# Kernel tuning notes

Hardware: AMD Instinct MI355X
Metric: run time of the kernel (lower is better)

## Reference

```python
import jax, jax.numpy as jnp
import numpy as np
import math

B, S, D, H = 2, 2048, 1024, 16
DK = D // H


def setup_inputs() -> dict:
    key = jax.random.key(0)
    ks = jax.random.split(key, 8)
    scale = 0.02
    f = lambda k, shape: jax.random.normal(k, shape, dtype=jnp.float32)
    causal = jnp.tril(jnp.ones((S, S), dtype=jnp.int32))  # [S,S]
    mask = jnp.broadcast_to(causal[None, None], (B, 1, S, S))
    return {
        "query": f(ks[0], (B, S, D)),
        "key_in": f(ks[1], (B, S, D)),
        "value": f(ks[2], (B, S, D)),
        "Wq": f(ks[3], (D, D)) * scale, "bq": jnp.zeros((D,), jnp.float32),
        "Wk": f(ks[4], (D, D)) * scale, "bk": jnp.zeros((D,), jnp.float32),
        "Wv": f(ks[5], (D, D)) * scale, "bv": jnp.zeros((D,), jnp.float32),
        "Wo": f(ks[6], (D, D)) * scale, "bo": jnp.zeros((D,), jnp.float32),
        "mask": mask,
    }


def reference(query, key_in, value, Wq, bq, Wk, bk, Wv, bv, Wo, bo, mask):
    # linear projections (torch Linear: x @ W.T + b), split into heads -> [B,H,S,DK]
    def proj(x, W, b):
        return (x @ W.T + b).reshape(B, -1, H, DK).transpose(0, 2, 1, 3)

    q = proj(query, Wq, bq)
    k = proj(key_in, Wk, bk)
    v = proj(value, Wv, bv)

    scores = jnp.einsum("bhqd,bhkd->bhqk", q, k) / math.sqrt(DK)  # [B,H,S,S]
    scores = jnp.where(mask.astype(bool), scores, -jnp.inf)
    attn = jax.nn.softmax(scores, axis=-1)
    x = jnp.einsum("bhqk,bhkd->bhqd", attn, v)  # [B,H,S,DK]
    x = x.transpose(0, 2, 1, 3).reshape(B, S, D)
    return x @ Wo.T + bo
```

## Files before the change

### kernel.cpp

```cpp
#include <hip/hip_runtime.h>
#include <hip/hip_bf16.h>

constexpr int Bc = 2, Sc = 2048, Dc = 1024, Hc = 16, DKc = 64;
constexpr int Nrows = Bc * Sc;

typedef short bf16x8 __attribute__((ext_vector_type(8)));
typedef float floatx4 __attribute__((ext_vector_type(4)));
typedef unsigned short u16x8 __attribute__((ext_vector_type(8)));

__device__ __forceinline__ short f2bf(float f) {
    union { float f; unsigned u; } v; v.f = f;
    unsigned r = v.u + 0x7FFFu + ((v.u >> 16) & 1u);
    return (short)(r >> 16);
}

__device__ __forceinline__ void gld16(const void* g, void* l) {
    __builtin_amdgcn_global_load_lds((const __attribute__((address_space(1))) unsigned int*)g,
                                     (__attribute__((address_space(3))) unsigned int*)l,
                                     16, 0, 0);
}

__global__ __launch_bounds__(256) void cvt_bf16(
        const float* __restrict__ s0, const float* __restrict__ s1, const float* __restrict__ s2,
        const float* __restrict__ s3, const float* __restrict__ s4, const float* __restrict__ s5,
        const float* __restrict__ s6,
        short* __restrict__ d0, short* __restrict__ d1, short* __restrict__ d2,
        short* __restrict__ d3, short* __restrict__ d4, short* __restrict__ d5,
        short* __restrict__ d6) {
    const float* src; short* dst; int n;
    switch (blockIdx.y) {
        case 0: src = s0; dst = d0; n = Nrows * Dc; break;
        case 1: src = s1; dst = d1; n = Nrows * Dc; break;
        case 2: src = s2; dst = d2; n = Nrows * Dc; break;
        case 3: src = s3; dst = d3; n = Dc * Dc; break;
        case 4: src = s4; dst = d4; n = Dc * Dc; break;
        case 5: src = s5; dst = d5; n = Dc * Dc; break;
        default: src = s6; dst = d6; n = Dc * Dc; break;
    }
    const int stride = gridDim.x * 256 * 8;
    for (int i = (blockIdx.x * 256 + threadIdx.x) * 8; i < n; i += stride) {
        const float4 a = *(const float4*)(src + i);
        const float4 b = *(const float4*)(src + i + 4);
        u16x8 o;
        o[0] = (unsigned short)f2bf(a.x); o[1] = (unsigned short)f2bf(a.y);
        o[2] = (unsigned short)f2bf(a.z); o[3] = (unsigned short)f2bf(a.w);
        o[4] = (unsigned short)f2bf(b.x); o[5] = (unsigned short)f2bf(b.y);
        o[6] = (unsigned short)f2bf(b.z); o[7] = (unsigned short)f2bf(b.w);
        *(u16x8*)(dst + i) = o;
    }
}

template <int BM>
__device__ __forceinline__ void gemm_body(const short* __restrict__ A,
                                          const short* __restrict__ W,
                                          const float* __restrict__ bias,
                                          void* __restrict__ Cout,
                                          int mode, short* As, short* Ws) {
    constexpr int K = Dc, BK = 64;
    constexpr int MB = BM / 16;
    constexpr int A_BLKS = MB * 2;
    constexpr int TOT = A_BLKS + 16;
    constexpr int PER_W = TOT / 4;
    constexpr int WMB = MB / 2;

    const int tid  = threadIdx.x;
    const int w    = tid >> 6;
    const int lane = tid & 63;
    const int quad = lane >> 4;
    const int l15  = lane & 15;
    const int rowBase = blockIdx.y * BM;
    const int colBase = blockIdx.x * 128;
    const int wm = w >> 1, wn = w & 1;

    floatx4 acc[WMB][4];
#pragma unroll
    for (int j = 0; j < WMB; ++j)
#pragma unroll
        for (int t = 0; t < 4; ++t) acc[j][t] = (floatx4){0.f, 0.f, 0.f, 0.f};

    for (int k0 = 0; k0 < K; k0 += BK) {
        __syncthreads();
#pragma unroll
        for (int i = 0; i < PER_W; ++i) {
            const int blk = w * PER_W + i;
            if (blk < A_BLKS) {
                const int mb = blk >> 1, kh = blk & 1;
                const short* g = A + (size_t)(rowBase + mb * 16 + l15) * K + k0 + kh * 32 + quad * 8;
                gld16(g, As + blk * 512);
            } else {
                const int b2 = blk - A_BLKS;
                const int nb = b2 >> 1, kh = b2 & 1;
                const short* g = W + (size_t)(colBase + nb * 16 + l15) * K + k0 + kh * 32 + quad * 8;
                gld16(g, Ws + b2 * 512);
            }
        }
        __syncthreads();

        bf16x8 af[WMB][2], wf[4][2];
#pragma unroll
        for (int j = 0; j < WMB; ++j)
#pragma unroll
            for (int kh = 0; kh < 2; ++kh)
                af[j][kh] = *(const bf16x8*)(As + ((wm * WMB + j) * 2 + kh) * 512 + lane * 8);
#pragma unroll
        for (int t = 0; t < 4; ++t)
#pragma unroll
            for (int kh = 0; kh < 2; ++kh)
                wf[t][kh] = *(const bf16x8*)(Ws + ((wn * 4 + t) * 2 + kh) * 512 + lane * 8);

#pragma unroll
        for (int kh = 0; kh < 2; ++kh)
#pragma unroll
            for (int j = 0; j < WMB; ++j)
#pragma unroll
                for (int t = 0; t < 4; ++t)
                    acc[j][t] = __builtin_amdgcn_mfma_f32_16x16x32_bf16(af[j][kh], wf[t][kh], acc[j][t], 0, 0, 0);
    }

#pragma unroll
    for (int j = 0; j < WMB; ++j) {
#pragma unroll
        for (int t = 0; t < 4; ++t) {
            const int col = colBase + wn * 64 + t * 16 + l15;
            const float bv = bias[col];
            const int row0 = rowBase + (wm * WMB + j) * 16 + quad * 4;
            if (mode == 0) {
                float* Co = (float*)Cout;
#pragma unroll
                for (int r = 0; r < 4; ++r)
                    Co[(size_t)(row0 + r) * Dc + col] = acc[j][t][r] + bv;
            } else {
                short* Co = (short*)Cout;
                const int b = row0 >> 11;
                const int ss0 = row0 & (Sc - 1);
                const int h = col >> 6, dk = col & 63;
                if (mode == 1) {
#pragma unroll
                    for (int r = 0; r < 4; ++r)
                        Co[(((size_t)(b * Hc + h)) * Sc + ss0 + r) * DKc + dk] = f2bf(acc[j][t][r] + bv);
                } else {
                    short4 pk;
                    pk.x = f2bf(acc[j][t][0] + bv); pk.y = f2bf(acc[j][t][1] + bv);
                    pk.z = f2bf(acc[j][t][2] + bv); pk.w = f2bf(acc[j][t][3] + bv);
                    *(short4*)(Co + (((size_t)(b * Hc + h)) * DKc + dk) * Sc + ss0) = pk;
                }
            }
        }
    }
}

__global__ __launch_bounds__(256) void gemm_qkv(
        const short* __restrict__ Aq, const short* __restrict__ Ak, const short* __restrict__ Av,
        const short* __restrict__ Wq, const short* __restrict__ Wk, const short* __restrict__ Wv,
        const float* __restrict__ bq, const float* __restrict__ bk, const float* __restrict__ bv,
        short* __restrict__ Oq, short* __restrict__ Ok, short* __restrict__ Ov) {
    __shared__ short As[128 * 64];
    __shared__ short Ws[128 * 64];
    const int z = blockIdx.z;
    const short* A = (z == 0) ? Aq : (z == 1) ? Ak : Av;
    const short* W = (z == 0) ? Wq : (z == 1) ? Wk : Wv;
    const float* bs = (z == 0) ? bq : (z == 1) ? bk : bv;
    short* O = (z == 0) ? Oq : (z == 1) ? Ok : Ov;
    gemm_body<128>(A, W, bs, O, (z == 2) ? 2 : 1, As, Ws);
}

__global__ __launch_bounds__(256) void gemm_out(const short* __restrict__ A,
                                                const short* __restrict__ W,
                                                const float* __restrict__ bias,
                                                float* __restrict__ C) {
    __shared__ short As[64 * 64];
    __shared__ short Ws[128 * 64];
    gemm_body<64>(A, W, bias, C, 0, As, Ws);
}

__global__ __launch_bounds__(256) void flash_attn_mfma(const short* __restrict__ Qg,
                                                       const short* __restrict__ Kg,
                                                       const short* __restrict__ Vtg,
                                                       short* __restrict__ X) {
    constexpr int LD = 88;
    __shared__ short Kt[64 * LD];
    __shared__ short Vl[64 * LD];
    __shared__ short Pl[4 * 16 * LD];

    const int bh = blockIdx.x;
    const int qt = blockIdx.y;
    const int tid  = threadIdx.x;
    const int w    = tid >> 6;
    const int lane = tid & 63;
    const int quad = lane >> 4;
    const int l15  = lane & 15;

    const short* Qb = Qg  + (size_t)bh * Sc * DKc;
    const short* Kb = Kg  + (size_t)bh * Sc * DKc;
    const short* Vb = Vtg + (size_t)bh * DKc * Sc;

    bf16x8 qf[2];
    {
        const short* qp = Qb + (size_t)(qt * 64 + w * 16 + l15) * DKc + quad * 8;
        qf[0] = *(const bf16x8*)(qp);
        qf[1] = *(const bf16x8*)(qp + 32);
    }

    floatx4 oacc[4];
#pragma unroll
    for (int t = 0; t < 4; ++t) oacc[t] = (floatx4){0.f, 0.f, 0.f, 0.f};
    float m_run[4], l_run[4];
#pragma unroll
    for (int r = 0; r < 4; ++r) { m_run[r] = -1e30f; l_run[r] = 0.f; }

    short* Pw = Pl + w * 16 * LD;

    for (int kt = 0; kt <= qt; ++kt) {
        __syncthreads();
#pragma unroll
        for (int i = 0; i < 2; ++i) {
            const int c = tid + 256 * i;
            const int ky = c >> 3, d8 = (c & 7) * 8;
            *(uint4*)&Kt[ky * LD + d8] = *(const uint4*)(Kb + (size_t)(kt * 64 + ky) * DKc + d8);
        }
#pragma unroll
        for (int i = 0; i < 2; ++i) {
            const int c = tid + 256 * i;
            const int dk = c >> 3, k8 = (c & 7) * 8;
            *(uint4*)&Vl[dk * LD + k8] = *(const uint4*)(Vb + (size_t)dk * Sc + kt * 64 + k8);
        }
        __syncthreads();

        floatx4 sacc[4];
#pragma unroll
        for (int t = 0; t < 4; ++t) sacc[t] = (floatx4){0.f, 0.f, 0.f, 0.f};
#pragma unroll
        for (int t = 0; t < 4; ++t)
#pragma unroll
            for (int kh = 0; kh < 2; ++kh) {
                const bf16x8 kf = *(const bf16x8*)&Kt[(t * 16 + l15) * LD + kh * 32 + quad * 8];
                sacc[t] = __builtin_amdgcn_mfma_f32_16x16x32_bf16(qf[kh], kf, sacc[t], 0, 0, 0);
            }

        const bool diag = (kt == qt);
#pragma unroll
        for (int t = 0; t < 4; ++t)
#pragma unroll
            for (int r = 0; r < 4; ++r) {
                float s = sacc[t][r] * 0.125f;
                if (diag && (t * 16 + l15) > (w * 16 + quad * 4 + r)) s = -1e30f;
                sacc[t][r] = s;
            }

        float mt[4];
#pragma unroll
        for (int r = 0; r < 4; ++r)
            mt[r] = fmaxf(fmaxf(sacc[0][r], sacc[1][r]), fmaxf(sacc[2][r], sacc[3][r]));
#pragma unroll
        for (int off = 1; off < 16; off <<= 1)
#pragma unroll
            for (int r = 0; r < 4; ++r) mt[r] = fmaxf(mt[r], __shfl_xor(mt[r], off));

        float mn[4], alpha[4];
#pragma unroll
        for (int r = 0; r < 4; ++r) {
            mn[r] = fmaxf(m_run[r], mt[r]);
            alpha[r] = __expf(m_run[r] - mn[r]);
            m_run[r] = mn[r];
        }

        float rs[4] = {0.f, 0.f, 0.f, 0.f};
#pragma unroll
        for (int t = 0; t < 4; ++t)
#pragma unroll
            for (int r = 0; r < 4; ++r) {
                const float p = __expf(sacc[t][r] - mn[r]);
                rs[r] += p;
                Pw[(quad * 4 + r) * LD + t * 16 + l15] = f2bf(p);
            }
#pragma unroll
        for (int off = 1; off < 16; off <<= 1)
#pragma unroll
            for (int r = 0; r < 4; ++r) rs[r] += __shfl_xor(rs[r], off);
#pragma unroll
        for (int r = 0; r < 4; ++r) l_run[r] = l_run[r] * alpha[r] + rs[r];
#pragma unroll
        for (int t = 0; t < 4; ++t)
#pragma unroll
            for (int r = 0; r < 4; ++r) oacc[t][r] *= alpha[r];

        __asm__ __volatile__("s_waitcnt lgkmcnt(0)" ::: "memory");

#pragma unroll
        for (int kh = 0; kh < 2; ++kh) {
            const bf16x8 pf = *(const bf16x8*)&Pw[l15 * LD + kh * 32 + quad * 8];
#pragma unroll
            for (int t = 0; t < 4; ++t) {
                const bf16x8 vf = *(const bf16x8*)&Vl[(t * 16 + l15) * LD + kh * 32 + quad * 8];
                oacc[t] = __builtin_amdgcn_mfma_f32_16x16x32_bf16(pf, vf, oacc[t], 0, 0, 0);
            }
        }
    }

    const int b = bh / Hc, h = bh % Hc;
#pragma unroll
    for (int t = 0; t < 4; ++t)
#pragma unroll
        for (int r = 0; r < 4; ++r) {
            const int srow = qt * 64 + w * 16 + quad * 4 + r;
            const int d = t * 16 + l15;
            X[((size_t)b * Sc + srow) * Dc + h * DKc + d] = f2bf(oacc[t][r] / l_run[r]);
        }
}

extern "C" void kernel_launch(void* const* d_in, const int* in_sizes, int n_in,
                              void* d_out, int out_size, void* d_ws, size_t ws_size,
                              hipStream_t stream) {
    const float* query  = (const float*)d_in[0];
    const float* key_in = (const float*)d_in[1];
    const float* value  = (const float*)d_in[2];
    const float* Wq = (const float*)d_in[3];
    const float* bq = (const float*)d_in[4];
    const float* Wk = (const float*)d_in[5];
    const float* bk = (const float*)d_in[6];
    const float* Wv = (const float*)d_in[7];
    const float* bv = (const float*)d_in[8];
    const float* Wo = (const float*)d_in[9];
    const float* bo = (const float*)d_in[10];

    constexpr size_t TEN = (size_t)Nrows * Dc;
    constexpr size_t WTEN = (size_t)Dc * Dc;
    short* qbf = (short*)d_ws;
    short* kbf = qbf + TEN;
    short* vbf = kbf + TEN;
    short* wqb = vbf + TEN;
    short* wkb = wqb + WTEN;
    short* wvb = wkb + WTEN;
    short* wob = wvb + WTEN;
    short* Qh  = wob + WTEN;
    short* Kh  = Qh + TEN;
    short* Vt  = Kh + TEN;
    short* Xb  = Vt + TEN;

    cvt_bf16<<<dim3(512, 7), 256, 0, stream>>>(query, key_in, value, Wq, Wk, Wv, Wo,
                                               qbf, kbf, vbf, wqb, wkb, wvb, wob);

    gemm_qkv<<<dim3(Dc / 128, Nrows / 128, 3), 256, 0, stream>>>(
        qbf, kbf, vbf, wqb, wkb, wvb, bq, bk, bv, Qh, Kh, Vt);

    flash_attn_mfma<<<dim3(Bc * Hc, Sc / 64), 256, 0, stream>>>(Qh, Kh, Vt, Xb);

    gemm_out<<<dim3(Dc / 128, Nrows / 64), 256, 0, stream>>>(Xb, wob, bo, (float*)d_out);
}
```

Baseline: 323.3 us.

## Compute transposed scores in attention to keep P in registers, async LDS loads

Restructures the flash attention kernel to compute S^T (K as the A operand, Q as B), so each lane holds a full query column and softmax reductions need only two cross-quad shuffles. P stays in registers as a zero-padded bf16x8 operand instead of going through LDS. K/V tiles are loaded with global_load_lds into an MFMA-fragment-native layout. Causal tiles are interleaved across blockIdx.y for load balance. Half of each PV MFMA's K dimension is zero padding, so MFMA work doubles in exchange for dropping the LDS round-trip and syncs.

```diff
diff --git a/kernel.cpp b/kernel.cpp
--- a/kernel.cpp
+++ b/kernel.cpp
@@ -5,6 +5,7 @@
 constexpr int Nrows = Bc * Sc;
 
 typedef short bf16x8 __attribute__((ext_vector_type(8)));
+typedef short bf16x4 __attribute__((ext_vector_type(4)));
 typedef float floatx4 __attribute__((ext_vector_type(4)));
 typedef unsigned short u16x8 __attribute__((ext_vector_type(8)));
 
@@ -177,13 +178,13 @@
                                                        const short* __restrict__ Kg,
                                                        const short* __restrict__ Vtg,
                                                        short* __restrict__ X) {
-    constexpr int LD = 88;
-    __shared__ short Kt[64 * LD];
-    __shared__ short Vl[64 * LD];
-    __shared__ short Pl[4 * 16 * LD];
+    __shared__ short Ks[8 * 512];
+    __shared__ short Vs[8 * 512];
 
     const int bh = blockIdx.x;
-    const int qt = blockIdx.y;
+    const int yy = blockIdx.y;
+    const int qt = (yy & 1) ? (31 - (yy >> 1)) : (yy >> 1);
+
     const int tid  = threadIdx.x;
     const int w    = tid >> 6;
     const int lane = tid & 63;
@@ -204,25 +205,23 @@
     floatx4 oacc[4];
 #pragma unroll
     for (int t = 0; t < 4; ++t) oacc[t] = (floatx4){0.f, 0.f, 0.f, 0.f};
-    float m_run[4], l_run[4];
-#pragma unroll
-    for (int r = 0; r < 4; ++r) { m_run[r] = -1e30f; l_run[r] = 0.f; }
-
-    short* Pw = Pl + w * 16 * LD;
+    float m_run = -1e30f, l_run = 0.f;
+    const int qloc = w * 16 + l15;
 
     for (int kt = 0; kt <= qt; ++kt) {
         __syncthreads();
 #pragma unroll
-        for (int i = 0; i < 2; ++i) {
-            const int c = tid + 256 * i;
-            const int ky = c >> 3, d8 = (c & 7) * 8;
-            *(uint4*)&Kt[ky * LD + d8] = *(const uint4*)(Kb + (size_t)(kt * 64 + ky) * DKc + d8);
-        }
-#pragma unroll
-        for (int i = 0; i < 2; ++i) {
-            const int c = tid + 256 * i;
-            const int dk = c >> 3, k8 = (c & 7) * 8;
-            *(uint4*)&Vl[dk * LD + k8] = *(const uint4*)(Vb + (size_t)dk * Sc + kt * 64 + k8);
+        for (int i = 0; i < 4; ++i) {
+            const int blk = w * 4 + i;
+            if (blk < 8) {
+                const int t = blk >> 1, kh = blk & 1;
+                gld16(Kb + (size_t)(kt * 64 + t * 16 + l15) * DKc + kh * 32 + quad * 8,
+                      Ks + blk * 512);
+            } else {
+                const int b2 = blk - 8, dt = b2 >> 1, t2 = b2 & 1;
+                gld16(Vb + (size_t)(dt * 16 + l15) * Sc + kt * 64 + t2 * 32 + quad * 8,
+                      Vs + b2 * 512);
+            }
         }
         __syncthreads();
 
@@ -233,8 +232,8 @@
         for (int t = 0; t < 4; ++t)
 #pragma unroll
             for (int kh = 0; kh < 2; ++kh) {
-                const bf16x8 kf = *(const bf16x8*)&Kt[(t * 16 + l15) * LD + kh * 32 + quad * 8];
-                sacc[t] = __builtin_amdgcn_mfma_f32_16x16x32_bf16(qf[kh], kf, sacc[t], 0, 0, 0);
+                const bf16x8 af = *(const bf16x8*)(Ks + (t * 2 + kh) * 512 + lane * 8);
+                sacc[t] = __builtin_amdgcn_mfma_f32_16x16x32_bf16(af, qf[kh], sacc[t], 0, 0, 0);
             }
 
         const bool diag = (kt == qt);
@@ -243,69 +242,69 @@
 #pragma unroll
             for (int r = 0; r < 4; ++r) {
                 float s = sacc[t][r] * 0.125f;
-                if (diag && (t * 16 + l15) > (w * 16 + quad * 4 + r)) s = -1e30f;
+                if (diag && (t * 16 + quad * 4 + r) > qloc) s = -1e30f;
                 sacc[t][r] = s;
             }
 
-        float mt[4];
-#pragma unroll
-        for (int r = 0; r < 4; ++r)
-            mt[r] = fmaxf(fmaxf(sacc[0][r], sacc[1][r]), fmaxf(sacc[2][r], sacc[3][r]));
-#pragma unroll
-        for (int off = 1; off < 16; off <<= 1)
-#pragma unroll
-            for (int r = 0; r < 4; ++r) mt[r] = fmaxf(mt[r], __shfl_xor(mt[r], off));
-
-        float mn[4], alpha[4];
-#pragma unroll
-        for (int r = 0; r < 4; ++r) {
-            mn[r] = fmaxf(m_run[r], mt[r]);
-            alpha[r] = __expf(m_run[r] - mn[r]);
-            m_run[r] = mn[r];
-        }
-
-        float rs[4] = {0.f, 0.f, 0.f, 0.f};
+        float mt = sacc[0][0];
 #pragma unroll
         for (int t = 0; t < 4; ++t)
 #pragma unroll
-            for (int r = 0; r < 4; ++r) {
-                const float p = __expf(sacc[t][r] - mn[r]);
-                rs[r] += p;
-                Pw[(quad * 4 + r) * LD + t * 16 + l15] = f2bf(p);
-            }
-#pragma unroll
-        for (int off = 1; off < 16; off <<= 1)
-#pragma unroll
-            for (int r = 0; r < 4; ++r) rs[r] += __shfl_xor(rs[r], off);
-#pragma unroll
-        for (int r = 0; r < 4; ++r) l_run[r] = l_run[r] * alpha[r] + rs[r];
-#pragma unroll
-        for (int t = 0; t < 4; ++t)
-#pragma unroll
-            for (int r = 0; r < 4; ++r) oacc[t][r] *= alpha[r];
-
-        __asm__ __volatile__("s_waitcnt lgkmcnt(0)" ::: "memory");
-
-#pragma unroll
-        for (int kh = 0; kh < 2; ++kh) {
-            const bf16x8 pf = *(const bf16x8*)&Pw[l15 * LD + kh * 32 + quad * 8];
-#pragma unroll
-            for (int t = 0; t < 4; ++t) {
-                const bf16x8 vf = *(const bf16x8*)&Vl[(t * 16 + l15) * LD + kh * 32 + quad * 8];
-                oacc[t] = __builtin_amdgcn_mfma_f32_16x16x32_bf16(pf, vf, oacc[t], 0, 0, 0);
-            }
-        }
-    }
-
-    const int b = bh / Hc, h = bh % Hc;
-#pragma unroll
-    for (int t = 0; t < 4; ++t)
-#pragma unroll
-        for (int r = 0; r < 4; ++r) {
-            const int srow = qt * 64 + w * 16 + quad * 4 + r;
-            const int d = t * 16 + l15;
-            X[((size_t)b * Sc + srow) * Dc + h * DKc + d] = f2bf(oacc[t][r] / l_run[r]);
-        }
+            for (int r = 0; r < 4; ++r) mt = fmaxf(mt, sacc[t][r]);
+        mt = fmaxf(mt, __shfl_xor(mt, 16));
+        mt = fmaxf(mt, __shfl_xor(mt, 32));
+
+        const float mn = fmaxf(m_run, mt);
+        const float alpha = __expf(m_run - mn);
+        m_run = mn;
+
+        float rs = 0.f;
+        bf16x8 pf[4];
+#pragma unroll
+        for (int t = 0; t < 4; ++t) {
+            float p0 = __expf(sacc[t][0] - mn);
+            float p1 = __expf(sacc[t][1] - mn);
+            float p2 = __expf(sacc[t][2] - mn);
+            float p3 = __expf(sacc[t][3] - mn);
+            rs += (p0 + p1) + (p2 + p3);
+            pf[t][0] = f2bf(p0); pf[t][1] = f2bf(p1);
+            pf[t][2] = f2bf(p2); pf[t][3] = f2bf(p3);
+            pf[t][4] = 0; pf[t][5] = 0; pf[t][6] = 0; pf[t][7] = 0;
+        }
+        rs += __shfl_xor(rs, 16);
+        rs += __shfl_xor(rs, 32);
+        l_run = l_run * alpha + rs;
+#pragma unroll
+        for (int dt = 0; dt < 4; ++dt) oacc[dt] *= alpha;
+
+#pragma unroll
+        for (int t = 0; t < 4; ++t) {
+            const int L2 = ((t & 1) * 2 + (quad >> 1)) * 16 + l15;
+            const int j0 = (quad & 1) * 4;
+#pragma unroll
+            for (int dt = 0; dt < 4; ++dt) {
+                const bf16x4 vv = *(const bf16x4*)(Vs + (dt * 2 + (t >> 1)) * 512 + L2 * 8 + j0);
+                bf16x8 vf;
+                vf[0] = vv[0]; vf[1] = vv[1]; vf[2] = vv[2]; vf[3] = vv[3];
+                vf[4] = 0; vf[5] = 0; vf[6] = 0; vf[7] = 0;
+                oacc[dt] = __builtin_amdgcn_mfma_f32_16x16x32_bf16(vf, pf[t], oacc[dt], 0, 0, 0);
+            }
+        }
+    }
+
+    const float inv = 1.0f / l_run;
+    const int b = bh >> 4, h = bh & 15;
+    const int qrow = qt * 64 + w * 16 + l15;
+    short* Xr = X + ((size_t)b * Sc + qrow) * Dc + h * DKc;
+#pragma unroll
+    for (int dt = 0; dt < 4; ++dt) {
+        short4 pk;
+        pk.x = f2bf(oacc[dt][0] * inv);
+        pk.y = f2bf(oacc[dt][1] * inv);
+        pk.z = f2bf(oacc[dt][2] * inv);
+        pk.w = f2bf(oacc[dt][3] * inv);
+        *(short4*)(Xr + dt * 16 + quad * 4) = pk;
+    }
 }
 
 extern "C" void kernel_launch(void* const* d_in, const int* in_sizes, int n_in,
```

After: 303.5 us. 1.07x faster.
